# Kernel tuning notes

Measured on AMD Instinct MI355X. Metric: run time of the kernel, lower is better.

Reference implementation:

```python
import jax, jax.numpy as jnp
import numpy as np

B, P, K, G_PER, F_IN, H, NECK = 16, 512, 32, 8, 59, 128, 512
N = B * P
E = N * K
G = N // G_PER
EPS = 1e-5


def setup_inputs() -> dict:
    rng = np.random.default_rng(0)
    f32 = lambda a: jnp.asarray(a, jnp.float32)
    x = f32(rng.standard_normal((N, F_IN)))
    pos = f32(rng.standard_normal((N, 3)) * 8.0)
    nrm = rng.standard_normal((N, 3))
    normal = f32(nrm / np.linalg.norm(nrm, axis=1, keepdims=True))
    # synthetic radius-graph edges: K neighbors per node within its own graph, incl. self edge
    nbr = rng.integers(0, P, size=(N, K))
    nbr[:, 0] = np.arange(N) % P  # self edge guarantees every dst segment is non-empty
    starts = np.repeat(np.arange(B) * P, P)
    src = jnp.asarray((starts[:, None] + nbr).reshape(-1), jnp.int32)
    dst = jnp.asarray(np.repeat(np.arange(N), K), jnp.int32)
    # raw (unnormalized but consecutive-run) residue labels, relabeled inside reference
    pool_batch = jnp.asarray(np.repeat(np.arange(G) * 3 + 7, G_PER), jnp.int32)
    mask_t = f32(np.repeat(rng.integers(0, 2, size=G), G_PER))
    def lin(i, o, bias=True):
        w = f32(rng.standard_normal((i, o)) / np.sqrt(i))
        return (w, f32(np.zeros(o))) if bias else w
    lin_w, lin_b = lin(F_IN, H)
    src_w = lin(F_IN, H, bias=False)
    dst_w = lin(F_IN, H, bias=False)
    posnn_w, posnn_b = lin(6, H)
    attnn_w, attnn_b = lin(H, H)
    neck_w, neck_b = lin(H, NECK)
    mlp1_w, mlp1_b = lin(NECK, 256)
    mlp2_w, mlp2_b = lin(256, 1)
    gb = lambda n: (f32(1.0 + 0.1 * rng.standard_normal(n)), f32(0.1 * rng.standard_normal(n)))
    posnn_g, posnn_bb = gb(H)
    attnn_g, attnn_bb = gb(H)
    neck_g, neck_bb = gb(NECK)
    mlp1_g, mlp1_bb = gb(256)
    return dict(x=x, pos=pos, normal=normal, mask_t=mask_t, pool_batch=pool_batch,
                src=src, dst=dst, lin_w=lin_w, lin_b=lin_b, src_w=src_w, dst_w=dst_w,
                posnn_w=posnn_w, posnn_b=posnn_b, posnn_g=posnn_g, posnn_bb=posnn_bb,
                attnn_w=attnn_w, attnn_b=attnn_b, attnn_g=attnn_g, attnn_bb=attnn_bb,
                neck_w=neck_w, neck_b=neck_b, neck_g=neck_g, neck_bb=neck_bb,
                mlp1_w=mlp1_w, mlp1_b=mlp1_b, mlp1_g=mlp1_g, mlp1_bb=mlp1_bb,
                mlp2_w=mlp2_w, mlp2_b=mlp2_b)


def bn_relu(h, g, b):
    # eval-mode BatchNorm1d (running_mean=0, running_var=1) + ReLU; Dropout is identity in eval
    return jax.nn.relu(h * (g / jnp.sqrt(1.0 + EPS)) + b)


def reference(x, pos, normal, mask_t, pool_batch, src, dst,
              lin_w, lin_b, src_w, dst_w,
              posnn_w, posnn_b, posnn_g, posnn_bb,
              attnn_w, attnn_b, attnn_g, attnn_bb,
              neck_w, neck_b, neck_g, neck_bb,
              mlp1_w, mlp1_b, mlp1_g, mlp1_bb,
              mlp2_w, mlp2_b):
    n = x.shape[0]
    # vectorized form of the per-element relabel loop: consecutive runs -> 0..G-1
    chg = jnp.concatenate([jnp.zeros((1,), jnp.int32),
                           (pool_batch[1:] != pool_batch[:-1]).astype(jnp.int32)])
    pb = jnp.cumsum(chg)
    # --- PointTransformerConv (gather -> pos_nn/attn_nn MLPs -> segment softmax -> scatter-add)
    v = x @ lin_w + lin_b                      # value projection [N,H]
    a_src = (x @ src_w)[src]                   # lin_src(x_j)   [E,H]
    a_dst = (x @ dst_w)[dst]                   # lin_dst(x_i)   [E,H]
    rel = jnp.concatenate([pos[dst] - pos[src], normal[dst] - normal[src]], axis=-1)  # [E,6]
    delta = bn_relu(rel @ posnn_w + posnn_b, posnn_g, posnn_bb)                       # [E,H]
    alpha = bn_relu((a_dst - a_src + delta) @ attnn_w + attnn_b, attnn_g, attnn_bb)   # [E,H]
    amax = jax.ops.segment_max(alpha, dst, num_segments=n)
    e = jnp.exp(alpha - amax[dst])
    den = jax.ops.segment_sum(e, dst, num_segments=n)
    attn = e / (den[dst] + 1e-16)              # per-destination softmax over neighbors
    h = jax.ops.segment_sum(attn * (v[src] + delta), dst, num_segments=n)  # [N,H]
    # --- neck, residue max-pool, head
    h = bn_relu(h @ neck_w + neck_b, neck_g, neck_bb)          # [N,512]
    gfeat = jax.ops.segment_max(h, pb, num_segments=G)         # global_max_pool  [G,512]
    gfeat = bn_relu(gfeat @ mlp1_w + mlp1_b, mlp1_g, mlp1_bb)  # [G,256]
    out = gfeat @ mlp2_w + mlp2_b                              # [G,1]
    mask_g = jax.ops.segment_max(mask_t, pb, num_segments=G)   # pooled mask_t
    # original does out[mask_t]; we zero non-selected rows to keep shapes static
    return out * (mask_g == 1.0).astype(out.dtype)[:, None]
```

## Files before the change

### kernel.cpp

```cpp
#include <hip/hip_runtime.h>
#include <hip/hip_bf16.h>
#include <cmath>

#define N_NODES 8192
#define F_INPUT 59
#define H 128
#define K 32
#define NECK 512
#define GPER 8
#define NG 1024
#define EPS_BN 1e-5f
#define DPITCH 136
#define XPITCH 72

typedef short bf16x8 __attribute__((ext_vector_type(8)));
typedef float f32x16 __attribute__((ext_vector_type(16)));

__device__ __forceinline__ void split_bf(float v, short& hi, short& lo) {
    unsigned u = __float_as_uint(v);
    float hif = __uint_as_float(u & 0xffff0000u);
    hi = (short)(u >> 16);
    lo = (short)(__float_as_uint(v - hif) >> 16);
}

__device__ __forceinline__ int bfrag_idx(int k, int c, int k16) {
    int ct = c >> 5, ln = c & 31;
    int s = k >> 4, hf = (k >> 3) & 1, kk = k & 7;
    return ((((ct * k16 + s) * 2 + hf) * 32 + ln) * 8 + kk);
}

__global__ __launch_bounds__(256) void prep_kernel(
    const float* __restrict__ lin_w,
    const float* __restrict__ src_w, const float* __restrict__ dst_w,
    const float* __restrict__ posnn_w,
    const float* __restrict__ attnn_w, const float* __restrict__ neck_w,
    short* __restrict__ w3hi, short* __restrict__ w3lo,
    short* __restrict__ pwhi, short* __restrict__ pwlo,
    short* __restrict__ awhi, short* __restrict__ awlo,
    short* __restrict__ nwhi, short* __restrict__ nwlo)
{
    const int b = blockIdx.x;
    if (b < F_INPUT) {
        const int c = threadIdx.x;
        if (c < H) {
            float a1 = 0.f, a2 = 0.f;
            for (int k = 0; k < H; k++) {
                float wa = attnn_w[k * H + c];
                a1 = fmaf(src_w[b * H + k], wa, a1);
                a2 = fmaf(dst_w[b * H + k], wa, a2);
            }
            short hi, lo; int idx;
            split_bf(lin_w[b * H + c], hi, lo);
            idx = bfrag_idx(b, c, 4);       w3hi[idx] = hi; w3lo[idx] = lo;
            split_bf(a1, hi, lo);
            idx = bfrag_idx(b, 128 + c, 4); w3hi[idx] = hi; w3lo[idx] = lo;
            split_bf(a2, hi, lo);
            idx = bfrag_idx(b, 256 + c, 4); w3hi[idx] = hi; w3lo[idx] = lo;
        }
    } else if (b == F_INPUT) {
        for (int t = threadIdx.x; t < 5 * 384; t += 256) {
            int k = F_INPUT + t / 384, c = t % 384;
            int idx = bfrag_idx(k, c, 4);
            w3hi[idx] = 0; w3lo[idx] = 0;
        }
    } else if (b == F_INPUT + 1) {
        for (int idx = threadIdx.x; idx < 2048; idx += 256) {
            int kk = idx & 7; int t = idx >> 3;
            int l2 = t & 31; t >>= 5;
            int hb = t & 1;  t >>= 1;
            int ct = t;
            int k = hb * 8 + kk, c = ct * 32 + l2;
            float wv = (k < 6) ? posnn_w[k * H + c] : 0.f;
            short hi, lo; split_bf(wv, hi, lo);
            pwhi[idx] = hi; pwlo[idx] = lo;
        }
    } else if (b < F_INPUT + 2 + 64) {
        int idx = (b - F_INPUT - 2) * 256 + threadIdx.x;
        int kk = idx & 7; int t = idx >> 3;
        int l2 = t & 31; t >>= 5;
        int hb = t & 1;  t >>= 1;
        int s  = t & 7;  t >>= 3;
        int c = t * 32 + l2, k = s * 16 + hb * 8 + kk;
        short hi, lo; split_bf(attnn_w[k * H + c], hi, lo);
        awhi[idx] = hi; awlo[idx] = lo;
    } else {
        int idx = (b - F_INPUT - 2 - 64) * 256 + threadIdx.x;
        int kk = idx & 7; int t = idx >> 3;
        int l2 = t & 31; t >>= 5;
        int hb = t & 1;  t >>= 1;
        int s  = t & 7;  t >>= 3;
        int c = t * 32 + l2, k = s * 16 + hb * 8 + kk;
        short hi, lo; split_bf(neck_w[k * NECK + c], hi, lo);
        nwhi[idx] = hi; nwlo[idx] = lo;
    }
}

__global__ __launch_bounds__(256) void proj_kernel(
    const float* __restrict__ x, const float* __restrict__ lin_b,
    const short* __restrict__ w3hi, const short* __restrict__ w3lo,
    float2* __restrict__ vx, float* __restrict__ xdW)
{
    const int n0 = blockIdx.x * 32;
    const int tid = threadIdx.x;
    const int wave = tid >> 6;
    const int lane = tid & 63;
    const int hf = lane >> 5;
    const int ln = lane & 31;

    __shared__ __align__(16) short xhi[32][XPITCH];
    __shared__ __align__(16) short xlo[32][XPITCH];

    for (int idx = tid; idx < 32 * F_INPUT; idx += 256) {
        int n = idx / F_INPUT, k = idx - n * F_INPUT;
        short hi, lo; split_bf(x[n0 * F_INPUT + idx], hi, lo);
        xhi[n][k] = hi; xlo[n][k] = lo;
    }
    if (tid < 32 * 5) {
        int n = tid / 5, k = F_INPUT + tid % 5;
        xhi[n][k] = 0; xlo[n][k] = 0;
    }
    __syncthreads();

    f32x16 acc[3];
    #pragma unroll
    for (int t = 0; t < 3; t++)
        #pragma unroll
        for (int r = 0; r < 16; r++) acc[t][r] = 0.f;

    #pragma unroll
    for (int s = 0; s < 4; s++) {
        bf16x8 ah = *(const bf16x8*)&xhi[ln][s * 16 + hf * 8];
        bf16x8 al = *(const bf16x8*)&xlo[ln][s * 16 + hf * 8];
        #pragma unroll
        for (int t = 0; t < 3; t++) {
            const int ct = wave + 4 * t;
            const int boff = (((ct * 4 + s) * 2 + hf) * 32 + ln) * 8;
            bf16x8 bh = *(const bf16x8*)&w3hi[boff];
            bf16x8 bl = *(const bf16x8*)&w3lo[boff];
            acc[t] = __builtin_amdgcn_mfma_f32_32x32x16_bf16(ah, bl, acc[t], 0, 0, 0);
            acc[t] = __builtin_amdgcn_mfma_f32_32x32x16_bf16(al, bh, acc[t], 0, 0, 0);
            acc[t] = __builtin_amdgcn_mfma_f32_32x32x16_bf16(ah, bh, acc[t], 0, 0, 0);
        }
    }
    const int c = wave * 32 + ln;
    const float lb = lin_b[c];
    #pragma unroll
    for (int r = 0; r < 16; r++) {
        int node = n0 + (r & 3) + 8 * (r >> 2) + 4 * hf;
        vx[node * H + c] = make_float2(acc[1][r], acc[0][r] + lb);
        xdW[node * H + c] = acc[2][r];
    }
}

__global__ __launch_bounds__(256) void edge_kernel(
    const float* __restrict__ pos, const float* __restrict__ normal,
    const int* __restrict__ src,
    const float2* __restrict__ vx, const float* __restrict__ xdW,
    const float* __restrict__ posnn_b, const float* __restrict__ posnn_g,
    const float* __restrict__ posnn_bb,
    const float* __restrict__ attnn_b,
    const float* __restrict__ attnn_g, const float* __restrict__ attnn_bb,
    const short* __restrict__ pwhi, const short* __restrict__ pwlo,
    const short* __restrict__ awhi, const short* __restrict__ awlo,
    unsigned* __restrict__ h2)
{
    const int i0 = blockIdx.x * 2;
    const int tid = threadIdx.x;
    const int wave = tid >> 6;
    const int lane = tid & 63;
    const int hf = lane >> 5;
    const int ln = lane & 31;

    __shared__ int srcs[2][K];
    __shared__ __align__(16) short relh[64][16];
    __shared__ __align__(16) short rell[64][16];
    __shared__ __align__(16) short dhi[64][DPITCH];
    __shared__ __align__(16) short dlo[64][DPITCH];

    if (tid < 64) {
        int n = tid >> 5, jj = tid & 31;
        int i = i0 + n;
        int s = src[i * K + jj];
        srcs[n][jj] = s;
        short h_, l_;
        #pragma unroll
        for (int k = 0; k < 3; k++) {
            split_bf(pos[i * 3 + k] - pos[s * 3 + k], h_, l_);
            relh[tid][k] = h_; rell[tid][k] = l_;
            split_bf(normal[i * 3 + k] - normal[s * 3 + k], h_, l_);
            relh[tid][k + 3] = h_; rell[tid][k + 3] = l_;
        }
        #pragma unroll
        for (int k = 6; k < 16; k++) { relh[tid][k] = 0; rell[tid][k] = 0; }
    }

    const int cc = wave * 32 + ln;
    const float ps  = posnn_g[cc] * rsqrtf(1.f + EPS_BN);
    const float pbn = fmaf(posnn_b[cc], ps, posnn_bb[cc]);
    const float as_ = attnn_g[cc] * rsqrtf(1.f + EPS_BN);
    const float abb = attnn_bb[cc];
    const float ab  = attnn_b[cc];

    const bf16x8 pbh = *(const bf16x8*)&pwhi[((wave * 2 + hf) * 32 + ln) * 8];
    const bf16x8 pbl = *(const bf16x8*)&pwlo[((wave * 2 + hf) * 32 + ln) * 8];

    __syncthreads();

    #pragma unroll
    for (int n = 0; n < 2; n++) {
        bf16x8 ah = *(const bf16x8*)&relh[32 * n + ln][hf * 8];
        bf16x8 al = *(const bf16x8*)&rell[32 * n + ln][hf * 8];
        f32x16 da;
        #pragma unroll
        for (int r = 0; r < 16; r++) da[r] = 0.f;
        da = __builtin_amdgcn_mfma_f32_32x32x16_bf16(ah, pbl, da, 0, 0, 0);
        da = __builtin_amdgcn_mfma_f32_32x32x16_bf16(al, pbh, da, 0, 0, 0);
        da = __builtin_amdgcn_mfma_f32_32x32x16_bf16(ah, pbh, da, 0, 0, 0);
        #pragma unroll
        for (int r = 0; r < 16; r++) {
            int j = (r & 3) + 8 * (r >> 2) + 4 * hf;
            float d = fmaxf(fmaf(da[r], ps, pbn), 0.f);
            short h_, l_; split_bf(d, h_, l_);
            dhi[32 * n + j][cc] = h_;
            dlo[32 * n + j][cc] = l_;
        }
    }
    __syncthreads();

    const short* whb = awhi + wave * 8 * 2 * 32 * 8;
    const short* wlb = awlo + wave * 8 * 2 * 32 * 8;

    #pragma clang loop unroll(disable)
    for (int n = 0; n < 2; n++) {
        const int i = i0 + n;
        f32x16 acc;
        #pragma unroll
        for (int r = 0; r < 16; r++) acc[r] = 0.f;
        #pragma unroll
        for (int s = 0; s < 8; s++) {
            bf16x8 ah = *(const bf16x8*)&dhi[32 * n + ln][s * 16 + hf * 8];
            bf16x8 al = *(const bf16x8*)&dlo[32 * n + ln][s * 16 + hf * 8];
            const int boff = ((s * 2 + hf) * 32 + ln) * 8;
            bf16x8 bh = *(const bf16x8*)&whb[boff];
            bf16x8 bl = *(const bf16x8*)&wlb[boff];
            acc = __builtin_amdgcn_mfma_f32_32x32x16_bf16(ah, bl, acc, 0, 0, 0);
            acc = __builtin_amdgcn_mfma_f32_32x32x16_bf16(al, bh, acc, 0, 0, 0);
            acc = __builtin_amdgcn_mfma_f32_32x32x16_bf16(ah, bh, acc, 0, 0, 0);
        }

        const float base = xdW[i * H + cc] + ab;
        float a[16], vv[16];
        float m = 0.f;
        #pragma unroll
        for (int r = 0; r < 16; r++) {
            int j = (r & 3) + 8 * (r >> 2) + 4 * hf;
            float2 g = vx[srcs[n][j] * H + cc];
            float al2 = acc[r] + base - g.x;
            float av = fmaxf(fmaf(al2, as_, abb), 0.f);
            a[r] = av; vv[r] = g.y;
            m = fmaxf(m, av);
        }
        m = fmaxf(m, __shfl_xor(m, 32, 64));
        float den = 0.f;
        #pragma unroll
        for (int r = 0; r < 16; r++) {
            float e = __expf(a[r] - m);
            a[r] = e; den += e;
        }
        den += __shfl_xor(den, 32, 64);
        const float inv = 1.f / (den + 1e-16f);

        float hsum = 0.f;
        #pragma unroll
        for (int r = 0; r < 16; r++) {
            int j = (r & 3) + 8 * (r >> 2) + 4 * hf;
            unsigned dh = (unsigned short)dhi[32 * n + j][cc];
            unsigned dl = (unsigned short)dlo[32 * n + j][cc];
            float dd = __uint_as_float(dh << 16) + __uint_as_float(dl << 16);
            hsum = fmaf(a[r], vv[r] + dd, hsum);
        }
        hsum += __shfl_xor(hsum, 32, 64);
        hsum *= inv;
        if (hf == 0) {
            unsigned u = __float_as_uint(hsum);
            unsigned hib = u & 0xffff0000u;
            unsigned lo = __float_as_uint(hsum - __uint_as_float(hib)) >> 16;
            h2[i * H + cc] = (lo << 16) | (u >> 16);
        }
    }
}

__global__ __launch_bounds__(256) void neck_head_kernel(
    const unsigned* __restrict__ h2,
    const short* __restrict__ nwhi, const short* __restrict__ nwlo,
    const float* __restrict__ neck_b, const float* __restrict__ neck_g,
    const float* __restrict__ neck_bb,
    const float* __restrict__ mask_t,
    const float* __restrict__ mlp1_w, const float* __restrict__ mlp1_b,
    const float* __restrict__ mlp1_g, const float* __restrict__ mlp1_bb,
    const float* __restrict__ mlp2_w, const float* __restrict__ mlp2_b,
    float* __restrict__ out)
{
    const int blk = blockIdx.x;
    const int n0 = blk * 32;
    const int tid = threadIdx.x;
    const int wave = tid >> 6;
    const int lane = tid & 63;
    const int hf = lane >> 5;
    const int ln = lane & 31;

    __shared__ __align__(16) short a_hi[32][DPITCH];
    __shared__ __align__(16) short a_lo[32][DPITCH];
    __shared__ float gfeat_l[4][NECK];
    __shared__ float red_l[4][4][256];

    for (int d = tid; d < 32 * H; d += 256) {
        unsigned u = h2[(n0 + (d >> 7)) * H + (d & 127)];
        a_hi[d >> 7][d & 127] = (short)(u & 0xffffu);
        a_lo[d >> 7][d & 127] = (short)(u >> 16);
    }
    __syncthreads();

    f32x16 acc[4];
    #pragma unroll
    for (int t = 0; t < 4; t++)
        #pragma unroll
        for (int r = 0; r < 16; r++) acc[t][r] = 0.f;

    #pragma unroll
    for (int s = 0; s < 8; s++) {
        bf16x8 ah = *(const bf16x8*)&a_hi[ln][s * 16 + hf * 8];
        bf16x8 al = *(const bf16x8*)&a_lo[ln][s * 16 + hf * 8];
        #pragma unroll
        for (int t = 0; t < 4; t++) {
            const int ct = wave * 4 + t;
            const int boff = (((ct * 8 + s) * 2 + hf) * 32 + ln) * 8;
            bf16x8 bh = *(const bf16x8*)&nwhi[boff];
            bf16x8 bl = *(const bf16x8*)&nwlo[boff];
            acc[t] = __builtin_amdgcn_mfma_f32_32x32x16_bf16(ah, bl, acc[t], 0, 0, 0);
            acc[t] = __builtin_amdgcn_mfma_f32_32x32x16_bf16(al, bh, acc[t], 0, 0, 0);
            acc[t] = __builtin_amdgcn_mfma_f32_32x32x16_bf16(ah, bh, acc[t], 0, 0, 0);
        }
    }

    #pragma unroll
    for (int t = 0; t < 4; t++) {
        const int c = wave * 128 + t * 32 + ln;
        const float s  = neck_g[c] * rsqrtf(1.f + EPS_BN);
        const float bnb = fmaf(neck_b[c], s, neck_bb[c]);
        #pragma unroll
        for (int g = 0; g < 4; g++) {
            float m = 0.f;
            #pragma unroll
            for (int q = 0; q < 4; q++)
                m = fmaxf(m, fmaf(acc[t][4 * g + q], s, bnb));
            m = fmaxf(m, __shfl_xor(m, 32, 64));
            if (hf == 0) gfeat_l[g][c] = m;
        }
    }
    __syncthreads();

    const int c4 = lane;
    float ph[4][4];
    #pragma unroll
    for (int g = 0; g < 4; g++)
        #pragma unroll
        for (int mm = 0; mm < 4; mm++) ph[g][mm] = 0.f;

    const int k0 = wave * 128;
    for (int k = 0; k < 128; k += 4) {
        float4 gv[4];
        #pragma unroll
        for (int g = 0; g < 4; g++) gv[g] = *(const float4*)&gfeat_l[g][k0 + k];
        #pragma unroll
        for (int kk = 0; kk < 4; kk++) {
            float w0 = mlp1_w[(k0 + k + kk) * 256 + c4];
            float w1 = mlp1_w[(k0 + k + kk) * 256 + c4 + 64];
            float w2 = mlp1_w[(k0 + k + kk) * 256 + c4 + 128];
            float w3 = mlp1_w[(k0 + k + kk) * 256 + c4 + 192];
            #pragma unroll
            for (int g = 0; g < 4; g++) {
                float gvk = (&gv[g].x)[kk];
                ph[g][0] = fmaf(gvk, w0, ph[g][0]);
                ph[g][1] = fmaf(gvk, w1, ph[g][1]);
                ph[g][2] = fmaf(gvk, w2, ph[g][2]);
                ph[g][3] = fmaf(gvk, w3, ph[g][3]);
            }
        }
    }
    #pragma unroll
    for (int g = 0; g < 4; g++)
        #pragma unroll
        for (int mm = 0; mm < 4; mm++)
            red_l[wave][g][c4 + 64 * mm] = ph[g][mm];
    __syncthreads();

    {
        const int g = wave;
        float part = 0.f;
        #pragma unroll
        for (int mm = 0; mm < 4; mm++) {
            const int c = c4 + 64 * mm;
            float sum = mlp1_b[c] + red_l[0][g][c] + red_l[1][g][c]
                      + red_l[2][g][c] + red_l[3][g][c];
            float s = mlp1_g[c] * rsqrtf(1.f + EPS_BN);
            float val = fmaxf(fmaf(sum, s, mlp1_bb[c]), 0.f);
            part = fmaf(val, mlp2_w[c], part);
        }
        #pragma unroll
        for (int off = 32; off > 0; off >>= 1) part += __shfl_xor(part, off, 64);
        if (lane == 0) {
            const int gg = blk * 4 + g;
            float mm = mask_t[gg * GPER];
            #pragma unroll
            for (int n = 1; n < GPER; n++) mm = fmaxf(mm, mask_t[gg * GPER + n]);
            out[gg] = (mm == 1.0f) ? (part + mlp2_b[0]) : 0.f;
        }
    }
}

extern "C" void kernel_launch(void* const* d_in, const int* in_sizes, int n_in,
                              void* d_out, int out_size, void* d_ws, size_t ws_size,
                              hipStream_t stream)
{
    const float* x        = (const float*)d_in[0];
    const float* pos      = (const float*)d_in[1];
    const float* normal   = (const float*)d_in[2];
    const float* mask_t   = (const float*)d_in[3];
    const int*   src      = (const int*)d_in[5];
    const float* lin_w    = (const float*)d_in[7];
    const float* lin_b    = (const float*)d_in[8];
    const float* src_w    = (const float*)d_in[9];
    const float* dst_w    = (const float*)d_in[10];
    const float* posnn_w  = (const float*)d_in[11];
    const float* posnn_b  = (const float*)d_in[12];
    const float* posnn_g  = (const float*)d_in[13];
    const float* posnn_bb = (const float*)d_in[14];
    const float* attnn_w  = (const float*)d_in[15];
    const float* attnn_b  = (const float*)d_in[16];
    const float* attnn_g  = (const float*)d_in[17];
    const float* attnn_bb = (const float*)d_in[18];
    const float* neck_w   = (const float*)d_in[19];
    const float* neck_b   = (const float*)d_in[20];
    const float* neck_g   = (const float*)d_in[21];
    const float* neck_bb  = (const float*)d_in[22];
    const float* mlp1_w   = (const float*)d_in[23];
    const float* mlp1_b   = (const float*)d_in[24];
    const float* mlp1_g   = (const float*)d_in[25];
    const float* mlp1_bb  = (const float*)d_in[26];
    const float* mlp2_w   = (const float*)d_in[27];
    const float* mlp2_b   = (const float*)d_in[28];

    float* ws = (float*)d_ws;
    float2*   vx   = (float2*)ws;
    float*    xdW  = (float*)(vx + (size_t)N_NODES * H);
    unsigned* h2   = (unsigned*)(xdW + (size_t)N_NODES * H);
    short*    w3hi = (short*)(h2 + (size_t)N_NODES * H);
    short*    w3lo = w3hi + 24576;
    short*    pwhi = w3lo + 24576;
    short*    pwlo = pwhi + 2048;
    short*    awhi = pwlo + 2048;
    short*    awlo = awhi + H * H;
    short*    nwhi = awlo + H * H;
    short*    nwlo = nwhi + H * NECK;

    prep_kernel<<<F_INPUT + 2 + 64 + 256, 256, 0, stream>>>(
        lin_w, src_w, dst_w, posnn_w, attnn_w, neck_w,
        w3hi, w3lo, pwhi, pwlo, awhi, awlo, nwhi, nwlo);
    proj_kernel<<<N_NODES / 32, 256, 0, stream>>>(x, lin_b, w3hi, w3lo, vx, xdW);
    edge_kernel<<<N_NODES / 2, 256, 0, stream>>>(pos, normal, src, vx, xdW,
                                                 posnn_b, posnn_g, posnn_bb,
                                                 attnn_b, attnn_g, attnn_bb,
                                                 pwhi, pwlo, awhi, awlo, h2);
    neck_head_kernel<<<N_NODES / 32, 256, 0, stream>>>(
        h2, nwhi, nwlo, neck_b, neck_g, neck_bb, mask_t,
        mlp1_w, mlp1_b, mlp1_g, mlp1_bb, mlp2_w, mlp2_b, (float*)d_out);
}
```

Before: 202.6 us.

## Fold attention BN scale into weights, keep delta in registers, drop lo-split MFMA

Folds the attention BatchNorm scale into the prepacked attnn weights and into the per-node projections, so the edge kernel no longer applies the affine per edge. The delta activations stay in registers for the aggregation step. Only a round-to-nearest bf16 copy goes to a repacked, fragment-ordered shared buffer as the MFMA A operand, which removes the lo plane and one of the three MFMAs per step. This cuts shared memory, LDS traffic and MFMA count, but lowers precision of the delta operand in the attention matmul to a single bf16.

```diff
diff --git a/kernel.cpp b/kernel.cpp
--- a/kernel.cpp
+++ b/kernel.cpp
@@ -12,6 +12,7 @@
 #define EPS_BN 1e-5f
 #define DPITCH 136
 #define XPITCH 72
+#define PLANE 272
 
 typedef short bf16x8 __attribute__((ext_vector_type(8)));
 typedef float f32x16 __attribute__((ext_vector_type(16)));
@@ -22,6 +23,10 @@
     hi = (short)(u >> 16);
     lo = (short)(__float_as_uint(v - hif) >> 16);
 }
+__device__ __forceinline__ short f2bfrn(float f) {
+    __hip_bfloat16 b = __float2bfloat16(f);
+    return *reinterpret_cast<short*>(&b);
+}
 
 __device__ __forceinline__ int bfrag_idx(int k, int c, int k16) {
     int ct = c >> 5, ln = c & 31;
@@ -33,7 +38,8 @@
     const float* __restrict__ lin_w,
     const float* __restrict__ src_w, const float* __restrict__ dst_w,
     const float* __restrict__ posnn_w,
-    const float* __restrict__ attnn_w, const float* __restrict__ neck_w,
+    const float* __restrict__ attnn_w, const float* __restrict__ attnn_g,
+    const float* __restrict__ neck_w,
     short* __restrict__ w3hi, short* __restrict__ w3lo,
     short* __restrict__ pwhi, short* __restrict__ pwlo,
     short* __restrict__ awhi, short* __restrict__ awlo,
@@ -81,7 +87,8 @@
         int hb = t & 1;  t >>= 1;
         int s  = t & 7;  t >>= 3;
         int c = t * 32 + l2, k = s * 16 + hb * 8 + kk;
-        short hi, lo; split_bf(attnn_w[k * H + c], hi, lo);
+        float scale = attnn_g[c] * rsqrtf(1.f + EPS_BN);
+        short hi, lo; split_bf(attnn_w[k * H + c] * scale, hi, lo);
         awhi[idx] = hi; awlo[idx] = lo;
     } else {
         int idx = (b - F_INPUT - 2 - 64) * 256 + threadIdx.x;
@@ -97,8 +104,10 @@
 
 __global__ __launch_bounds__(256) void proj_kernel(
     const float* __restrict__ x, const float* __restrict__ lin_b,
+    const float* __restrict__ attnn_g, const float* __restrict__ attnn_b,
+    const float* __restrict__ attnn_bb,
     const short* __restrict__ w3hi, const short* __restrict__ w3lo,
-    float2* __restrict__ vx, float* __restrict__ xdW)
+    float2* __restrict__ vx, float* __restrict__ xdb)
 {
     const int n0 = blockIdx.x * 32;
     const int tid = threadIdx.x;
@@ -143,23 +152,23 @@
         }
     }
     const int c = wave * 32 + ln;
-    const float lb = lin_b[c];
+    const float lb  = lin_b[c];
+    const float as_ = attnn_g[c] * rsqrtf(1.f + EPS_BN);
+    const float cbn = fmaf(attnn_b[c], as_, attnn_bb[c]);
     #pragma unroll
     for (int r = 0; r < 16; r++) {
         int node = n0 + (r & 3) + 8 * (r >> 2) + 4 * hf;
-        vx[node * H + c] = make_float2(acc[1][r], acc[0][r] + lb);
-        xdW[node * H + c] = acc[2][r];
+        vx[node * H + c] = make_float2(as_ * acc[1][r], acc[0][r] + lb);
+        xdb[node * H + c] = fmaf(acc[2][r], as_, cbn);
     }
 }
 
 __global__ __launch_bounds__(256) void edge_kernel(
     const float* __restrict__ pos, const float* __restrict__ normal,
     const int* __restrict__ src,
-    const float2* __restrict__ vx, const float* __restrict__ xdW,
+    const float2* __restrict__ vx, const float* __restrict__ xdb,
     const float* __restrict__ posnn_b, const float* __restrict__ posnn_g,
     const float* __restrict__ posnn_bb,
-    const float* __restrict__ attnn_b,
-    const float* __restrict__ attnn_g, const float* __restrict__ attnn_bb,
     const short* __restrict__ pwhi, const short* __restrict__ pwlo,
     const short* __restrict__ awhi, const short* __restrict__ awlo,
     unsigned* __restrict__ h2)
@@ -172,10 +181,9 @@
     const int ln = lane & 31;
 
     __shared__ int srcs[2][K];
-    __shared__ __align__(16) short relh[64][16];
-    __shared__ __align__(16) short rell[64][16];
-    __shared__ __align__(16) short dhi[64][DPITCH];
-    __shared__ __align__(16) short dlo[64][DPITCH];
+    __shared__ __align__(16) short relh[4 * PLANE];
+    __shared__ __align__(16) short rell[4 * PLANE];
+    __shared__ __align__(16) short dpk[32 * PLANE];
 
     if (tid < 64) {
         int n = tid >> 5, jj = tid & 31;
@@ -183,33 +191,37 @@
         int s = src[i * K + jj];
         srcs[n][jj] = s;
         short h_, l_;
+        const int b0 = (n * 2) * PLANE + jj * 8;
+        const int b1 = (n * 2 + 1) * PLANE + jj * 8;
         #pragma unroll
         for (int k = 0; k < 3; k++) {
             split_bf(pos[i * 3 + k] - pos[s * 3 + k], h_, l_);
-            relh[tid][k] = h_; rell[tid][k] = l_;
+            relh[b0 + k] = h_; rell[b0 + k] = l_;
             split_bf(normal[i * 3 + k] - normal[s * 3 + k], h_, l_);
-            relh[tid][k + 3] = h_; rell[tid][k + 3] = l_;
-        }
-        #pragma unroll
-        for (int k = 6; k < 16; k++) { relh[tid][k] = 0; rell[tid][k] = 0; }
+            relh[b0 + k + 3] = h_; rell[b0 + k + 3] = l_;
+        }
+        #pragma unroll
+        for (int k = 6; k < 8; k++) { relh[b0 + k] = 0; rell[b0 + k] = 0; }
+        #pragma unroll
+        for (int k = 0; k < 8; k++) { relh[b1 + k] = 0; rell[b1 + k] = 0; }
     }
 
     const int cc = wave * 32 + ln;
     const float ps  = posnn_g[cc] * rsqrtf(1.f + EPS_BN);
     const float pbn = fmaf(posnn_b[cc], ps, posnn_bb[cc]);
-    const float as_ = attnn_g[cc] * rsqrtf(1.f + EPS_BN);
-    const float abb = attnn_bb[cc];
-    const float ab  = attnn_b[cc];
 
     const bf16x8 pbh = *(const bf16x8*)&pwhi[((wave * 2 + hf) * 32 + ln) * 8];
     const bf16x8 pbl = *(const bf16x8*)&pwlo[((wave * 2 + hf) * 32 + ln) * 8];
 
-    __syncthreads();
-
+    const int dbase = ((cc >> 4) * 2 + ((cc >> 3) & 1)) * PLANE + (cc & 7);
+
+    __syncthreads();
+
+    float dreg[2][16];
     #pragma unroll
     for (int n = 0; n < 2; n++) {
-        bf16x8 ah = *(const bf16x8*)&relh[32 * n + ln][hf * 8];
-        bf16x8 al = *(const bf16x8*)&rell[32 * n + ln][hf * 8];
+        bf16x8 ah = *(const bf16x8*)&relh[(n * 2 + hf) * PLANE + ln * 8];
+        bf16x8 al = *(const bf16x8*)&rell[(n * 2 + hf) * PLANE + ln * 8];
         f32x16 da;
         #pragma unroll
         for (int r = 0; r < 16; r++) da[r] = 0.f;
@@ -220,9 +232,8 @@
         for (int r = 0; r < 16; r++) {
             int j = (r & 3) + 8 * (r >> 2) + 4 * hf;
             float d = fmaxf(fmaf(da[r], ps, pbn), 0.f);
-            short h_, l_; split_bf(d, h_, l_);
-            dhi[32 * n + j][cc] = h_;
-            dlo[32 * n + j][cc] = l_;
+            dreg[n][r] = d;
+            dpk[n * 16 * PLANE + dbase + j * 8] = f2bfrn(d);
         }
     }
     __syncthreads();
@@ -238,25 +249,22 @@
         for (int r = 0; r < 16; r++) acc[r] = 0.f;
         #pragma unroll
         for (int s = 0; s < 8; s++) {
-            bf16x8 ah = *(const bf16x8*)&dhi[32 * n + ln][s * 16 + hf * 8];
-            bf16x8 al = *(const bf16x8*)&dlo[32 * n + ln][s * 16 + hf * 8];
+            bf16x8 ah = *(const bf16x8*)&dpk[((n * 8 + s) * 2 + hf) * PLANE + ln * 8];
             const int boff = ((s * 2 + hf) * 32 + ln) * 8;
             bf16x8 bh = *(const bf16x8*)&whb[boff];
             bf16x8 bl = *(const bf16x8*)&wlb[boff];
+            acc = __builtin_amdgcn_mfma_f32_32x32x16_bf16(ah, bh, acc, 0, 0, 0);
             acc = __builtin_amdgcn_mfma_f32_32x32x16_bf16(ah, bl, acc, 0, 0, 0);
-            acc = __builtin_amdgcn_mfma_f32_32x32x16_bf16(al, bh, acc, 0, 0, 0);
-            acc = __builtin_amdgcn_mfma_f32_32x32x16_bf16(ah, bh, acc, 0, 0, 0);
-        }
-
-        const float base = xdW[i * H + cc] + ab;
+        }
+
+        const float base = xdb[i * H + cc];
         float a[16], vv[16];
         float m = 0.f;
         #pragma unroll
         for (int r = 0; r < 16; r++) {
             int j = (r & 3) + 8 * (r >> 2) + 4 * hf;
             float2 g = vx[srcs[n][j] * H + cc];
-            float al2 = acc[r] + base - g.x;
-            float av = fmaxf(fmaf(al2, as_, abb), 0.f);
+            float av = fmaxf(acc[r] + base - g.x, 0.f);
             a[r] = av; vv[r] = g.y;
             m = fmaxf(m, av);
         }
@@ -272,13 +280,8 @@
 
         float hsum = 0.f;
         #pragma unroll
-        for (int r = 0; r < 16; r++) {
-            int j = (r & 3) + 8 * (r >> 2) + 4 * hf;
-            unsigned dh = (unsigned short)dhi[32 * n + j][cc];
-            unsigned dl = (unsigned short)dlo[32 * n + j][cc];
-            float dd = __uint_as_float(dh << 16) + __uint_as_float(dl << 16);
-            hsum = fmaf(a[r], vv[r] + dd, hsum);
-        }
+        for (int r = 0; r < 16; r++)
+            hsum = fmaf(a[r], vv[r] + dreg[n][r], hsum);
         hsum += __shfl_xor(hsum, 32, 64);
         hsum *= inv;
         if (hf == 0) {
@@ -453,8 +456,8 @@
 
     float* ws = (float*)d_ws;
     float2*   vx   = (float2*)ws;
-    float*    xdW  = (float*)(vx + (size_t)N_NODES * H);
-    unsigned* h2   = (unsigned*)(xdW + (size_t)N_NODES * H);
+    float*    xdb  = (float*)(vx + (size_t)N_NODES * H);
+    unsigned* h2   = (unsigned*)(xdb + (size_t)N_NODES * H);
     short*    w3hi = (short*)(h2 + (size_t)N_NODES * H);
     short*    w3lo = w3hi + 24576;
     short*    pwhi = w3lo + 24576;
@@ -465,12 +468,12 @@
     short*    nwlo = nwhi + H * NECK;
 
     prep_kernel<<<F_INPUT + 2 + 64 + 256, 256, 0, stream>>>(
-        lin_w, src_w, dst_w, posnn_w, attnn_w, neck_w,
+        lin_w, src_w, dst_w, posnn_w, attnn_w, attnn_g, neck_w,
         w3hi, w3lo, pwhi, pwlo, awhi, awlo, nwhi, nwlo);
-    proj_kernel<<<N_NODES / 32, 256, 0, stream>>>(x, lin_b, w3hi, w3lo, vx, xdW);
-    edge_kernel<<<N_NODES / 2, 256, 0, stream>>>(pos, normal, src, vx, xdW,
+    proj_kernel<<<N_NODES / 32, 256, 0, stream>>>(x, lin_b, attnn_g, attnn_b, attnn_bb,
+                                                  w3hi, w3lo, vx, xdb);
+    edge_kernel<<<N_NODES / 2, 256, 0, stream>>>(pos, normal, src, vx, xdb,
                                                  posnn_b, posnn_g, posnn_bb,
-                                                 attnn_b, attnn_g, attnn_bb,
                                                  pwhi, pwlo, awhi, awlo, h2);
     neck_head_kernel<<<N_NODES / 32, 256, 0, stream>>>(
         h2, nwhi, nwlo, neck_b, neck_g, neck_bb, mask_t,
```

New measurement: 249.1 us. 1.23x slower.
